# Kernel optimization log

Hardware: AMD Instinct MI355X
Metric: run time of the kernel (lower is better)

Reference implementation:

```python
import jax, jax.numpy as jnp
import numpy as np

ANGRES = 5  # u = v = angRes, n = 25


def _l2norm(x, axis):
    n = jnp.sqrt(jnp.sum(x * x, axis=axis, keepdims=True))
    return x / jnp.maximum(n, 1e-12)  # matches torch F.normalize eps


def _cos_attn(qm, km, vm):
    # qm: (b, M, K), km: (b, K, M), vm: (b, M, K)
    q = _l2norm(qm, -1)
    k = _l2norm(km, -2)
    att = jax.nn.softmax(q @ k, axis=-1)  # (b, M, M)
    return att @ vm


def _af_attn(x, u, v):  # AngularFrequencyAttention: b c (u v) h w -> b (c u) (h v w)
    b, c, n, h, w = x.shape
    t = x.reshape(b, c, u, v, h, w)
    qm = t.transpose(0, 1, 2, 4, 3, 5).reshape(b, c * u, h * v * w)   # (b,c,u,h,v,w)
    km = t.transpose(0, 4, 3, 5, 1, 2).reshape(b, h * v * w, c * u)   # (b,h,v,w,c,u)
    o = _cos_attn(qm, km, qm)
    o = o.reshape(b, c, u, h, v, w).transpose(0, 1, 2, 4, 3, 5).reshape(b, c, n, h, w)
    return o + x


def _sa_attn(x, u, v):  # SpatialAngularAttention: b c (u v) h w -> b (h u) (c v w)
    b, c, n, h, w = x.shape
    t = x.reshape(b, c, u, v, h, w)
    qm = t.transpose(0, 4, 2, 1, 3, 5).reshape(b, h * u, c * v * w)   # (b,h,u,c,v,w)
    km = t.transpose(0, 1, 3, 5, 4, 2).reshape(b, c * v * w, h * u)   # (b,c,v,w,h,u)
    o = _cos_attn(qm, km, qm)
    o = o.reshape(b, h, u, c, v, w).transpose(0, 3, 2, 4, 1, 5).reshape(b, c, n, h, w)
    return o + x


def _sf_attn(x, u, v):  # SpatialFrequencyAttention: b c (u v) h w -> b (c h) (w u v)
    b, c, n, h, w = x.shape
    t = x.reshape(b, c, u, v, h, w)
    qm = t.transpose(0, 1, 4, 5, 2, 3).reshape(b, c * h, w * u * v)   # (b,c,h,w,u,v)
    km = t.transpose(0, 5, 2, 3, 1, 4).reshape(b, w * u * v, c * h)   # (b,w,u,v,c,h)
    o = _cos_attn(qm, km, qm)
    o = o.reshape(b, c, h, w, u, v).transpose(0, 1, 4, 5, 2, 3).reshape(b, c, n, h, w)
    return o + x


def _layernorm(x, g, bta, eps=1e-5):
    mu = jnp.mean(x, -1, keepdims=True)
    var = jnp.mean(jnp.square(x - mu), -1, keepdims=True)
    return (x - mu) * jax.lax.rsqrt(var + eps) * g + bta


def setup_inputs() -> dict:
    key = jax.random.key(0)
    k0, k1, k2 = jax.random.split(key, 3)
    b, c, n, h, w = 4, 64, 25, 48, 48
    x = jax.random.normal(k0, (b, c, n, h, w), dtype=jnp.float32)
    gamma = jnp.ones((3 * c,), dtype=jnp.float32)
    beta = jnp.zeros((3 * c,), dtype=jnp.float32)
    w1 = jax.random.normal(k1, (3 * c, c), dtype=jnp.float32) * 0.02
    w2 = jax.random.normal(k2, (c, c), dtype=jnp.float32) * 0.02
    return {"x": x, "gamma": gamma, "beta": beta, "w1": w1, "w2": w2}


def reference(x, gamma, beta, w1, w2):
    u = v = ANGRES
    b, c, n, h, w = x.shape
    sf = _sf_attn(x, u, v)
    af = _af_attn(x, u, v)
    sa = _sa_attn(x, u, v)
    cat = jnp.concatenate([sf, af, sa], axis=1)            # (b, 3c, n, h, w)
    f = cat.transpose(0, 3, 4, 2, 1).reshape(b * h * w, n, 3 * c)
    y = _layernorm(f, gamma, beta)
    y = jax.nn.relu(y @ w1) @ w2                            # (bhw, n, c); dropout p=0.01 is eval-identity
    out = y.reshape(b, h, w, n, c).transpose(0, 4, 3, 1, 2) + x
    return out
```

## Files before the change

kernel.cpp:

```cpp
#include <hip/hip_runtime.h>
#include <stdint.h>

typedef __attribute__((ext_vector_type(8))) short bf16x8;
typedef __attribute__((ext_vector_type(4))) float f32x4;

__device__ __forceinline__ float b2f(short s) {
  union { unsigned u; float f; } a; a.u = ((unsigned)(unsigned short)s) << 16; return a.f;
}
__device__ __forceinline__ short f2b(float f) {
  union { float f; unsigned u; } a; a.f = f;
  unsigned r = a.u + 0x7fffu + ((a.u >> 16) & 1u);
  return (short)(r >> 16);
}
__device__ __forceinline__ void gload16(const void* g, void* l) {
  __builtin_amdgcn_global_load_lds((__attribute__((address_space(1))) void*)g,
                                   (__attribute__((address_space(3))) void*)l, 16, 0, 0);
}

#define SWZ(row, col) ((col) ^ (((row) & 7) << 3))

__global__ __launch_bounds__(256) void permute_sf_k(const float* __restrict__ x,
                                                    short* __restrict__ Q,
                                                    float* __restrict__ inv) {
  __shared__ float buf[4][1200];
  int wave = threadIdx.x >> 6, lane = threadIdx.x & 63;
  int gr = blockIdx.x * 4 + wave;
  int b = gr / 3072, m = gr - b * 3072;
  int c = m / 48, hh = m - c * 48;
  const float* xb = x + (long)(b * 64 + c) * 57600 + hh * 48;
  for (int uv = 0; uv < 25; ++uv)
    if (lane < 48) buf[wave][uv * 48 + lane] = xb[uv * 2304 + lane];
  __syncthreads();
  short* Qr = Q + (long)gr * 1280;
  float ss = 0.f;
  for (int k = lane; k < 1280; k += 64) {
    float v = 0.f;
    if (k < 1200) { int wv = k / 25, uv = k - wv * 25; v = buf[wave][uv * 48 + wv]; }
    ss += v * v;
    Qr[k] = f2b(v);
  }
  #pragma unroll
  for (int o = 32; o >= 1; o >>= 1) ss += __shfl_xor(ss, o, 64);
  if (lane == 0) inv[gr] = 1.0f / fmaxf(sqrtf(ss), 1e-12f);
}

__global__ __launch_bounds__(256) void permtr_all_k(const float* __restrict__ x,
    short* __restrict__ Qaf, short* __restrict__ QTaf,
    short* __restrict__ Qsa, short* __restrict__ QTsa,
    float* __restrict__ ssaf, float* __restrict__ sssa) {
  __shared__ short t[32][33];
  int bid = blockIdx.x;
  int isAF = (bid < 17280);
  int M, Mp, Kp, kt, mt, b;
  short *Q, *QT; float* ss;
  if (isAF) { M = 320; Mp = 384; Kp = 11520; kt = bid % 360; int r = bid / 360; mt = r % 12; b = r / 12;
              Q = Qaf; QT = QTaf; ss = ssaf; }
  else { int id = bid - 17280; M = 240; Mp = 256; Kp = 15360; kt = id % 480; int r = id / 480; mt = r % 8; b = r / 8;
         Q = Qsa; QT = QTsa; ss = sssa; }
  int k0 = kt * 32, m0 = mt * 32;
  int tx = threadIdx.x & 31, ty = threadIdx.x >> 5;
  const float* xb = x + (long)b * 3686400;
  #pragma unroll
  for (int i = 0; i < 32; i += 8) {
    int m = m0 + ty + i, k = k0 + tx;
    float v = 0.f;
    if (m < M) {
      int q1 = k / 240, r2 = k - q1 * 240;
      int v5 = r2 / 48, wv = r2 - v5 * 48;
      int a1 = m / 5, u = m - a1 * 5;
      long xi = isAF ? ((long)a1 * 25 + u * 5 + v5) * 2304 + q1 * 48 + wv
                     : ((long)q1 * 25 + u * 5 + v5) * 2304 + a1 * 48 + wv;
      v = xb[xi];
    }
    t[ty + i][tx] = f2b(v);
  }
  __syncthreads();
  long Qb = (long)b * Mp * Kp;
  #pragma unroll
  for (int i = 0; i < 32; i += 8)
    Q[Qb + (long)(m0 + ty + i) * Kp + k0 + tx] = t[ty + i][tx];
  #pragma unroll
  for (int i = 0; i < 32; i += 8)
    QT[Qb + (long)(k0 + ty + i) * Mp + m0 + tx] = t[tx][ty + i];
  if (threadIdx.x < 32 && m0 + (int)threadIdx.x < M) {
    float s = 0.f;
    #pragma unroll
    for (int k = 0; k < 32; ++k) { float f = b2f(t[threadIdx.x][k]); s += f * f; }
    atomicAdd(&ss[b * Mp + m0 + threadIdx.x], s);
  }
}

__global__ __launch_bounds__(256) void transpose_k(const short* __restrict__ in, short* __restrict__ out,
                                                   int R, int C) {
  __shared__ short t[32][33];
  long base = (long)blockIdx.z * R * C;
  int c0 = blockIdx.x * 32, r0 = blockIdx.y * 32;
  int tx = threadIdx.x & 31, ty = threadIdx.x >> 5;
  #pragma unroll
  for (int i = 0; i < 32; i += 8)
    t[ty + i][tx] = in[base + (long)(r0 + ty + i) * C + c0 + tx];
  __syncthreads();
  #pragma unroll
  for (int i = 0; i < 32; i += 8)
    out[base + (long)(c0 + ty + i) * R + r0 + tx] = t[tx][ty + i];
}

__global__ __launch_bounds__(256, 2) void gemm1_tri_k(const short* __restrict__ Q,
                                                      const float* __restrict__ invn,
                                                      short* __restrict__ att,
                                                      float* __restrict__ rowsum) {
  __shared__ short sm[32768];
  int tid = threadIdx.x, wave = tid >> 6, lane = tid & 63;
  int la = lane & 15, lb = lane >> 4;
  int bat = blockIdx.z;
  int bx = blockIdx.x, yt = 0, rem = bx;
  while (rem >= 24 - yt) { rem -= 24 - yt; ++yt; }
  int xt = yt + rem;
  const short* Qb = Q + (long)bat * 3932160L;
  const float* inv = invn + (long)bat * 3072;
  int row0 = yt * 128, col0 = xt * 128;
  f32x4 acc[4][4] = {};
  int wr = wave >> 1, wc = wave & 1;
  int rloc = tid >> 3, cbase = (tid & 7) * 8;
  int ldsoff = tid * 8;

  const short *pA[4], *pB[4];
  #pragma unroll
  for (int p = 0; p < 4; ++p) {
    int row = p * 32 + rloc;
    int sc = SWZ(row, cbase);
    pA[p] = Qb + (long)(row0 + row) * 1280 + sc;
    pB[p] = Qb + (long)(col0 + row) * 1280 + sc;
  }

  #define TRI_STAGE(KT, BUF) { \
    short* Asb = sm + (BUF) * 16384; \
    short* Bsb = Asb + 8192; \
    _Pragma("unroll") \
    for (int p = 0; p < 4; ++p) { \
      gload16(pA[p] + (KT) * 64, (void*)(Asb + p * 2048 + ldsoff)); \
      gload16(pB[p] + (KT) * 64, (void*)(Bsb + p * 2048 + ldsoff)); \
    } }
  #define TRI_COMP(BUF) { \
    const short* Asb = sm + (BUF) * 16384; \
    const short* Bsb = Asb + 8192; \
    _Pragma("unroll") \
    for (int kk = 0; kk < 64; kk += 32) { \
      bf16x8 av[4], bv[4]; \
      _Pragma("unroll") \
      for (int m = 0; m < 4; ++m) \
        av[m] = *(const bf16x8*)&Asb[(wr * 64 + m * 16 + la) * 64 + SWZ(la, kk + lb * 8)]; \
      _Pragma("unroll") \
      for (int nn = 0; nn < 4; ++nn) \
        bv[nn] = *(const bf16x8*)&Bsb[(wc * 64 + nn * 16 + la) * 64 + SWZ(la, kk + lb * 8)]; \
      _Pragma("unroll") \
      for (int m = 0; m < 4; ++m) \
        _Pragma("unroll") \
        for (int nn = 0; nn < 4; ++nn) \
          acc[m][nn] = __builtin_amdgcn_mfma_f32_16x16x32_bf16(av[m], bv[nn], acc[m][nn], 0, 0, 0); \
    } }

  TRI_STAGE(0, 0)
  for (int kt = 0; kt < 19; ++kt) {
    TRI_STAGE(kt + 1, (kt + 1) & 1)
    asm volatile("s_waitcnt vmcnt(8)" ::: "memory");
    __builtin_amdgcn_s_barrier();
    TRI_COMP(kt & 1)
    asm volatile("" ::: "memory");
    __builtin_amdgcn_s_barrier();
  }
  asm volatile("s_waitcnt vmcnt(0)" ::: "memory");
  __builtin_amdgcn_s_barrier();
  TRI_COMP(1)
  asm volatile("" ::: "memory");
  __builtin_amdgcn_s_barrier();

  short* staged = sm;
  #pragma unroll
  for (int m = 0; m < 4; ++m) {
    #pragma unroll
    for (int nn = 0; nn < 4; ++nn) {
      int cl = wc * 64 + nn * 16 + la;
      float ic = inv[col0 + cl];
      #pragma unroll
      for (int j = 0; j < 4; ++j) {
        int rl = wr * 64 + m * 16 + lb * 4 + j;
        staged[rl * 136 + cl] = f2b(__expf(acc[m][nn][j] * inv[row0 + rl] * ic));
      }
    }
  }
  __syncthreads();
  short* attb = att + (long)bat * 9437184L;
  float* rsb = rowsum + (long)bat * 3072;
  {
    int r = tid >> 1, half = tid & 1;
    short* dst = attb + (long)(row0 + r) * 3072 + col0 + half * 64;
    const short* src = &staged[r * 136 + half * 64];
    float s = 0.f;
    #pragma unroll
    for (int q = 0; q < 8; ++q) {
      bf16x8 v = *(const bf16x8*)&src[q * 8];
      *(bf16x8*)&dst[q * 8] = v;
      #pragma unroll
      for (int jj = 0; jj < 8; ++jj) s += b2f(v[jj]);
    }
    s += __shfl_xor(s, 1, 64);
    if (half == 0) atomicAdd(&rsb[row0 + r], s);
  }
  if (xt != yt) {
    int c = tid >> 1, half = tid & 1;
    short* dst = attb + (long)(col0 + c) * 3072 + row0 + half * 64;
    float s = 0.f;
    #pragma unroll
    for (int q = 0; q < 8; ++q) {
      bf16x8 o;
      #pragma unroll
      for (int jj = 0; jj < 8; ++jj) {
        o[jj] = staged[(half * 64 + q * 8 + jj) * 136 + c];
        s += b2f(o[jj]);
      }
      *(bf16x8*)&dst[q * 8] = o;
    }
    s += __shfl_xor(s, 1, 64);
    if (half == 0) atomicAdd(&rsb[col0 + c], s);
  }
}

__global__ __launch_bounds__(256, 2) void gemm_s_all_k(
    const short* __restrict__ Aaf, const short* __restrict__ Asa,
    float* __restrict__ Sfaf, float* __restrict__ Sfsa)
{
  __shared__ short sm[32768];
  int bid = blockIdx.x;
  const short* A; float* Sf;
  int lda, ktotal, ksper, ldc, row0, col0, bat, kc;
  long sA, sS;
  if (bid < 288) {
    int txy = bid % 9, z = bid / 9;
    col0 = (txy % 3) * 128; row0 = (txy / 3) * 128;
    bat = z / 8; kc = z % 8;
    lda = 11520; ktotal = 180; ksper = 23; ldc = 384;
    sA = 4423680L; sS = 147456L; A = Aaf; Sf = Sfaf;
  } else {
    int id = bid - 288;
    int txy = id % 4, z = id / 4;
    col0 = (txy % 2) * 128; row0 = (txy / 2) * 128;
    bat = z / 16; kc = z % 16;
    lda = 15360; ktotal = 240; ksper = 15; ldc = 256;
    sA = 3932160L; sS = 65536L; A = Asa; Sf = Sfsa;
  }
  int tid = threadIdx.x;
  int wave = tid >> 6, lane = tid & 63;
  int la = lane & 15, lb = lane >> 4;
  const short* Ab = A + (long)bat * sA;
  int kb = kc * ksper, ke = min(ktotal, kb + ksper);
  int L = ke - kb;
  f32x4 acc[4][4] = {};
  int wr = wave >> 1, wc = wave & 1;
  int rloc = tid >> 3, cbase = (tid & 7) * 8;
  int ldsoff = tid * 8;

  const short *pA[4], *pB[4];
  #pragma unroll
  for (int p = 0; p < 4; ++p) {
    int row = p * 32 + rloc;
    int sc = SWZ(row, cbase);
    pA[p] = Ab + (long)(row0 + row) * lda + sc;
    pB[p] = Ab + (long)(col0 + row) * lda + sc;
  }

  #define GS_STAGE(KT, BUF) { \
    short* Asb = sm + (BUF) * 16384; \
    short* Bsb = Asb + 8192; \
    _Pragma("unroll") \
    for (int p = 0; p < 4; ++p) { \
      gload16(pA[p] + (KT) * 64, (void*)(Asb + p * 2048 + ldsoff)); \
      gload16(pB[p] + (KT) * 64, (void*)(Bsb + p * 2048 + ldsoff)); \
    } }
  #define GS_COMP(BUF) { \
    const short* Asb = sm + (BUF) * 16384; \
    const short* Bsb = Asb + 8192; \
    _Pragma("unroll") \
    for (int kk = 0; kk < 64; kk += 32) { \
      bf16x8 av[4], bv[4]; \
      _Pragma("unroll") \
      for (int m = 0; m < 4; ++m) \
        av[m] = *(const bf16x8*)&Asb[(wr * 64 + m * 16 + la) * 64 + SWZ(la, kk + lb * 8)]; \
      _Pragma("unroll") \
      for (int nn = 0; nn < 4; ++nn) \
        bv[nn] = *(const bf16x8*)&Bsb[(wc * 64 + nn * 16 + la) * 64 + SWZ(la, kk + lb * 8)]; \
      _Pragma("unroll") \
      for (int m = 0; m < 4; ++m) \
        _Pragma("unroll") \
        for (int nn = 0; nn < 4; ++nn) \
          acc[m][nn] = __builtin_amdgcn_mfma_f32_16x16x32_bf16(av[m], bv[nn], acc[m][nn], 0, 0, 0); \
    } }

  GS_STAGE(kb, 0)
  for (int t = 0; t < L - 1; ++t) {
    GS_STAGE(kb + t + 1, (t + 1) & 1)
    asm volatile("s_waitcnt vmcnt(8)" ::: "memory");
    __builtin_amdgcn_s_barrier();
    GS_COMP(t & 1)
    asm volatile("" ::: "memory");
    __builtin_amdgcn_s_barrier();
  }
  asm volatile("s_waitcnt vmcnt(0)" ::: "memory");
  __builtin_amdgcn_s_barrier();
  GS_COMP((L - 1) & 1)

  float* Sb = Sf + (long)bat * sS;
  #pragma unroll
  for (int m = 0; m < 4; ++m) {
    int gr0 = row0 + wr * 64 + m * 16 + lb * 4;
    #pragma unroll
    for (int nn = 0; nn < 4; ++nn) {
      int gc = col0 + wc * 64 + nn * 16 + la;
      #pragma unroll
      for (int j = 0; j < 4; ++j)
        atomicAdd(&Sb[(long)(gr0 + j) * ldc + gc], acc[m][nn][j]);
    }
  }
}

__global__ __launch_bounds__(256) void softmax_all_k(
    const float* __restrict__ Sfaf, const float* __restrict__ Sfsa,
    const float* __restrict__ ssaf, const float* __restrict__ sssa,
    short* __restrict__ attaf, short* __restrict__ attsa)
{
  int wave = threadIdx.x >> 6, lane = threadIdx.x & 63;
  int rid = blockIdx.x * 4 + wave;
  int row, b, Mv, Mp; const float *Sf, *ss; short* att;
  if (rid < 1280) { row = rid % 320; b = rid / 320; Mv = 320; Mp = 384; Sf = Sfaf; ss = ssaf; att = attaf; }
  else { int id = rid - 1280; row = id % 240; b = id / 240; Mv = 240; Mp = 256; Sf = Sfsa; ss = sssa; att = attsa; }
  long sS = (long)Mp * Mp;
  const float* Sr = Sf + (long)b * sS + (long)row * Mp;
  const float* ssb = ss + b * Mp;
  float inv_i = rsqrtf(fmaxf(ssb[row], 1e-24f));
  float ev[6] = {0.f, 0.f, 0.f, 0.f, 0.f, 0.f};
  float sum = 0.f;
  #pragma unroll
  for (int q = 0; q < 6; ++q) {
    int j = q * 64 + lane;
    if (j < Mv) {
      float e = __expf(Sr[j] * inv_i * rsqrtf(fmaxf(ssb[j], 1e-24f)));
      ev[q] = e; sum += e;
    }
  }
  #pragma unroll
  for (int o = 32; o >= 1; o >>= 1) sum += __shfl_xor(sum, o, 64);
  float rden = 1.0f / sum;
  short* ar = att + (long)b * sS + (long)row * Mp;
  #pragma unroll
  for (int q = 0; q < 6; ++q) {
    int j = q * 64 + lane;
    if (j < Mp) ar[j] = (j < Mv) ? f2b(ev[q] * rden) : (short)0;
  }
}

__global__ __launch_bounds__(512) void gemm2sf_k(const short* __restrict__ A,
                                                 const short* __restrict__ B,
                                                 const float* __restrict__ rowsum,
                                                 short* __restrict__ F) {
  __shared__ short sm[65536];
  int tid = threadIdx.x;
  int wave = tid >> 6, lane = tid & 63;
  int la = lane & 15, lb = lane >> 4;
  int wr = wave >> 2, wc = wave & 3;
  int wk;
  { int xcd = blockIdx.x & 7, j = blockIdx.x >> 3; wk = xcd * 30 + j; }
  int yt = wk % 12, rem = wk / 12;
  int xt = rem % 5, bat = rem / 5;
  const short* Ab = A + (long)bat * 9437184L;
  const short* Bb = B + (long)bat * 3932160L;
  int rloc = tid >> 3;
  int cbase = (tid & 7) * 8;
  int sc = cbase ^ ((rloc & 7) << 3);
  const short *pAg[4], *pBg[4];
  #pragma unroll
  for (int g = 0; g < 4; ++g) {
    pAg[g] = Ab + (long)(rloc * 48 + yt * 4 + g) * 3072 + sc;
    pBg[g] = Bb + (long)(xt * 256 + g * 64 + rloc) * 3072 + sc;
  }
  f32x4 acc[8][4] = {};

  #pragma unroll
  for (int g = 0; g < 4; ++g) {
    gload16(pAg[g], (void*)(sm + g * 4096 + tid * 8));
    gload16(pBg[g], (void*)(sm + 16384 + g * 4096 + tid * 8));
  }
  asm volatile("s_waitcnt vmcnt(0)" ::: "memory");
  __builtin_amdgcn_s_barrier();

  #define G2_PHASE(MH, KK, LOADB) { \
    if (LOADB) { \
      _Pragma("unroll") \
      for (int nn = 0; nn < 4; ++nn) \
        bv[nn] = *(const bf16x8*)&Bsb[(wc * 64 + nn * 16 + la) * 64 + SWZ(la, (KK) + lb * 8)]; \
    } \
    _Pragma("unroll") \
    for (int m = 0; m < 4; ++m) \
      av[m] = *(const bf16x8*)&Asb[(wr * 128 + (MH) * 64 + m * 16 + la) * 64 + SWZ(la, (KK) + lb * 8)]; \
    __builtin_amdgcn_s_setprio(1); \
    _Pragma("unroll") \
    for (int m = 0; m < 4; ++m) \
      _Pragma("unroll") \
      for (int nn = 0; nn < 4; ++nn) \
        acc[(MH) * 4 + m][nn] = __builtin_amdgcn_mfma_f32_16x16x32_bf16(av[m], bv[nn], acc[(MH) * 4 + m][nn], 0, 0, 0); \
    __builtin_amdgcn_s_setprio(0); \
  }

  for (int t = 0; t < 48; ++t) {
    const short* Asb = sm + (t & 1) * 32768;
    const short* Bsb = Asb + 16384;
    short* An = sm + ((t + 1) & 1) * 32768;
    short* Bn = An + 16384;
    int k1 = (t + 1) * 64;
    bool pf = (t < 47);
    bf16x8 av[4], bv[4];

    asm volatile("s_waitcnt vmcnt(2)" ::: "memory");
    __builtin_amdgcn_s_barrier();
    if (pf) { gload16(pBg[0] + k1, (void*)(Bn + tid * 8));
              gload16(pBg[1] + k1, (void*)(Bn + 4096 + tid * 8)); }
    G2_PHASE(0, 0, 1)
    asm volatile("s_waitcnt vmcnt(2)" ::: "memory");
    __builtin_amdgcn_s_barrier();
    if (pf) { gload16(pBg[2] + k1, (void*)(Bn + 8192 + tid * 8));
              gload16(pBg[3] + k1, (void*)(Bn + 12288 + tid * 8)); }
    G2_PHASE(1, 0, 0)
    asm volatile("s_waitcnt vmcnt(4)" ::: "memory");
    __builtin_amdgcn_s_barrier();
    if (pf) { gload16(pAg[0] + k1, (void*)(An + tid * 8));
              gload16(pAg[2] + k1, (void*)(An + 8192 + tid * 8)); }
    G2_PHASE(0, 32, 1)
    asm volatile("s_waitcnt vmcnt(6)" ::: "memory");
    __builtin_amdgcn_s_barrier();
    if (pf) { gload16(pAg[1] + k1, (void*)(An + 4096 + tid * 8));
              gload16(pAg[3] + k1, (void*)(An + 12288 + tid * 8)); }
    G2_PHASE(1, 32, 0)
  }
  __syncthreads();

  const float* rsb = rowsum + (long)bat * 3072;
  float rs[8][4];
  #pragma unroll
  for (int m = 0; m < 8; ++m) {
    int sub = wr * 2 + (m >> 2);
    #pragma unroll
    for (int j = 0; j < 4; ++j) {
      int cc = (m & 3) * 16 + lb * 4 + j;
      rs[m][j] = 1.0f / rsb[cc * 48 + yt * 4 + sub];
    }
  }
  short* staged = sm;
  #pragma unroll
  for (int m = 0; m < 8; ++m) {
    int sub = wr * 2 + (m >> 2);
    #pragma unroll
    for (int nn = 0; nn < 4; ++nn) {
      int gcl = wc * 64 + nn * 16 + la;
      int chunk = gcl * 4 + sub;
      int key = (gcl & 7) << 3;
      short4 o;
      o.x = f2b(acc[m][nn][0] * rs[m][0]); o.y = f2b(acc[m][nn][1] * rs[m][1]);
      o.z = f2b(acc[m][nn][2] * rs[m][2]); o.w = f2b(acc[m][nn][3] * rs[m][3]);
      *(short4*)&staged[chunk * 64 + (((m & 3) * 16 + lb * 4) ^ key)] = o;
    }
  }
  __syncthreads();
  #pragma unroll
  for (int i = 0; i < 16; ++i) {
    int chunk = i * 64 + (tid >> 3);
    int part = tid & 7;
    int gcl = chunk >> 2, sub = chunk & 3;
    int key = (gcl & 7) << 3;
    bf16x8 v = *(const bf16x8*)&staged[chunk * 64 + ((part * 8) ^ key)];
    int gc = xt * 256 + gcl;
    if (gc < 1200) {
      int hh = yt * 4 + sub;
      int wv = gc / 25, nidx = gc - wv * 25;
      long base = (((long)(bat * 48 + hh) * 48 + wv) * 25 + nidx) * 192 + part * 8;
      *(bf16x8*)&F[base] = v;
    }
  }
}

__global__ __launch_bounds__(256) void gemm2_afsa_k(
    const short* __restrict__ attaf, const short* __restrict__ QTaf,
    const short* __restrict__ attsa, const short* __restrict__ QTsa,
    short* __restrict__ F)
{
  __shared__ short sm[20480];
  short* As = sm;
  short* Bs = sm + 4096;
  int bid = blockIdx.x;
  int isAF = (bid < 900);
  int NX, NY, LDA, KST, wk;
  const short *A, *B; long SA, SB;
  if (isAF) {
    NX = 45; NY = 5; LDA = 384; KST = 6; SA = 147456L; SB = 4423680L; A = attaf; B = QTaf;
    int xcd = bid & 7, j = bid >> 3;
    wk = (xcd < 4) ? xcd * 113 + j : 4 * 113 + (xcd - 4) * 112 + j;
  } else {
    NX = 60; NY = 4; LDA = 256; KST = 4; SA = 65536L; SB = 3932160L; A = attsa; B = QTsa;
    int id = bid - 900;
    int xcd = id & 7, j = id >> 3;
    wk = xcd * 120 + j;
  }
  int yt = wk % NY, rem = wk / NY;
  int xt = rem % NX, bat = rem / NX;
  int tid = threadIdx.x, wave = tid >> 6, lane = tid & 63;
  int la = lane & 15, lb = lane >> 4;
  const short* Ab = A + (long)bat * SA;
  const short* Bb = B + (long)bat * SB;
  f32x4 acc[4][4] = {};
  int rloc = tid >> 3, cbase = (tid & 7) * 8;
  int ldsoff = tid * 8;

  const short *pA[2], *pB[8];
  #pragma unroll
  for (int p = 0; p < 2; ++p) {
    int r = p * 32 + rloc;
    int sc = SWZ(r, cbase);
    int rowg = isAF ? (r * 5 + yt) : (yt * 64 + r);
    pA[p] = Ab + (long)rowg * LDA + sc;
  }
  #pragma unroll
  for (int p = 0; p < 8; ++p) {
    int rb = p * 32 + rloc;
    int sc = SWZ(rb, cbase);
    int rowg;
    if (isAF) rowg = xt * 256 + rb;
    else { int c = rb & 63, g = rb >> 6; rowg = c * 240 + xt * 4 + g; }
    pB[p] = Bb + (long)rowg * LDA + sc;
  }

  for (int kt = 0; kt < KST; ++kt) {
    #pragma unroll
    for (int p = 0; p < 2; ++p)
      gload16(pA[p] + kt * 64, (void*)(As + p * 2048 + ldsoff));
    #pragma unroll
    for (int p = 0; p < 8; ++p)
      gload16(pB[p] + kt * 64, (void*)(Bs + p * 2048 + ldsoff));
    __syncthreads();
    #pragma unroll
    for (int kk = 0; kk < 64; kk += 32) {
      bf16x8 av[4], bv[4];
      #pragma unroll
      for (int m = 0; m < 4; ++m)
        av[m] = *(const bf16x8*)&As[(m * 16 + la) * 64 + SWZ(la, kk + lb * 8)];
      #pragma unroll
      for (int nn = 0; nn < 4; ++nn)
        bv[nn] = *(const bf16x8*)&Bs[(wave * 64 + nn * 16 + la) * 64 + SWZ(la, kk + lb * 8)];
      #pragma unroll
      for (int m = 0; m < 4; ++m)
        #pragma unroll
        for (int nn = 0; nn < 4; ++nn)
          acc[m][nn] = __builtin_amdgcn_mfma_f32_16x16x32_bf16(av[m], bv[nn], acc[m][nn], 0, 0, 0);
    }
    __syncthreads();
  }

  short* staged = sm;
  #pragma unroll
  for (int m = 0; m < 4; ++m) {
    #pragma unroll
    for (int nn = 0; nn < 4; ++nn) {
      if (!isAF) {
        #pragma unroll
        for (int j = 0; j < 4; ++j)
          staged[((m * 16 + lb * 4 + j) * 4 + wave) * 72 + nn * 16 + la] = f2b(acc[m][nn][j]);
      } else {
        short4 o;
        o.x = f2b(acc[m][nn][0]); o.y = f2b(acc[m][nn][1]);
        o.z = f2b(acc[m][nn][2]); o.w = f2b(acc[m][nn][3]);
        *(short4*)&staged[(wave * 64 + nn * 16 + la) * 72 + m * 16 + lb * 4] = o;
      }
    }
  }
  __syncthreads();

  #pragma unroll
  for (int rd = 0; rd < 8; ++rd) {
    int chunk = rd * 32 + (tid >> 3);
    int part = tid & 7;
    bf16x8 v = *(const bf16x8*)&staged[chunk * 72 + part * 8];
    long base; bool ok = true;
    if (isAF) {
      int gc = xt * 256 + chunk;
      int hh = gc / 240, r2 = gc - hh * 240, v5 = r2 / 48, wv = r2 - v5 * 48;
      base = (((long)(bat * 48 + hh) * 48 + wv) * 25 + yt * 5 + v5) * 192 + 64 + part * 8;
    } else {
      int r = chunk >> 2, g = chunk & 3;
      int gr = yt * 64 + r; ok = (gr < 240);
      int hh = gr / 5, u = gr - hh * 5;
      int r2 = xt * 4 + g, v5 = r2 / 48, wv = r2 - v5 * 48;
      base = (((long)(bat * 48 + hh) * 48 + wv) * 25 + u * 5 + v5) * 192 + 128 + part * 8;
    }
    if (ok) *(bf16x8*)&F[base] = v;
  }
}

__global__ __launch_bounds__(256) void prep_w_k(const float* __restrict__ w1, const float* __restrict__ w2,
                                                short* __restrict__ w1t, short* __restrict__ w2t) {
  int idx = blockIdx.x * 256 + threadIdx.x;
  if (idx < 12288) {
    int i = idx / 64, j = idx - i * 64;
    w1t[j * 192 + i] = f2b(w1[idx]);
  } else if (idx < 16384) {
    int k = idx - 12288;
    int i = k / 64, j = k - i * 64;
    w2t[j * 64 + i] = f2b(w2[k]);
  }
}

__global__ __launch_bounds__(256) void ln_mlp_mfma_k(
    const short* __restrict__ F, const float* __restrict__ x,
    const float* __restrict__ gamma, const float* __restrict__ beta,
    const short* __restrict__ w1t, const short* __restrict__ w2t,
    float* __restrict__ out)
{
  int n = blockIdx.x, hh = blockIdx.y, b = blockIdx.z;
  __shared__ short A1[48 * 200];
  __shared__ float xs[64 * 49];
  __shared__ __align__(16) char pool[19584];
  short* Fs = (short*)pool;
  short* Y1 = (short*)pool;
  float* Y2 = (float*)(pool + 6912);
  int tid = threadIdx.x, wave = tid >> 6, lane = tid & 63;
  int la = lane & 15, lb = lane >> 4;
  long Fb0 = ((long)(b * 48 + hh) * 1200 + n) * 192;
  long xb = (long)b * 3686400 + (long)n * 2304 + hh * 48;

  #pragma unroll
  for (int it = 0; it < 5; ++it) {
    int ci = tid + 256 * it;
    if (ci < 1152) {
      int r = ci / 24, q = ci - r * 24;
      gload16(&F[Fb0 + (long)r * 4800 + q * 8], (void*)(Fs + ci * 8));
    }
  }
  {
    int ch = tid >> 2, qq = tid & 3;
    const float* xr = x + xb + (long)ch * 57600 + qq * 12;
    #pragma unroll
    for (int i = 0; i < 12; ++i) xs[ch * 49 + qq * 12 + i] = xr[i];
  }
  __syncthreads();

  float g0 = gamma[lane], g1 = gamma[lane + 64], g2 = gamma[lane + 128];
  float bt0 = beta[lane], bt1 = beta[lane + 64], bt2 = beta[lane + 128];
  #pragma unroll 4
  for (int rr = 0; rr < 12; ++rr) {
    int r = wave * 12 + rr;
    float xv = xs[lane * 49 + r];
    float v0 = b2f(Fs[r * 192 + lane]) + xv;
    float v1 = b2f(Fs[r * 192 + lane + 64]) + xv;
    float v2 = b2f(Fs[r * 192 + lane + 128]) + xv;
    float s = v0 + v1 + v2;
    #pragma unroll
    for (int o = 32; o >= 1; o >>= 1) s += __shfl_xor(s, o, 64);
    float mu = s * (1.f / 192.f);
    float d0 = v0 - mu, d1 = v1 - mu, d2 = v2 - mu;
    float q = d0 * d0 + d1 * d1 + d2 * d2;
    #pragma unroll
    for (int o = 32; o >= 1; o >>= 1) q += __shfl_xor(q, o, 64);
    float rsq = rsqrtf(q * (1.f / 192.f) + 1e-5f);
    A1[r * 200 + lane]       = f2b(d0 * rsq * g0 + bt0);
    A1[r * 200 + lane + 64]  = f2b(d1 * rsq * g1 + bt1);
    A1[r * 200 + lane + 128] = f2b(d2 * rsq * g2 + bt2);
  }
  __syncthreads();

  f32x4 acc1[3] = {};
  #pragma unroll
  for (int ks = 0; ks < 6; ++ks) {
    bf16x8 bv = *(const bf16x8*)&w1t[(wave * 16 + la) * 192 + ks * 32 + lb * 8];
    #pragma unroll
    for (int m = 0; m < 3; ++m) {
      bf16x8 av = *(const bf16x8*)&A1[(m * 16 + la) * 200 + ks * 32 + lb * 8];
      acc1[m] = __builtin_amdgcn_mfma_f32_16x16x32_bf16(av, bv, acc1[m], 0, 0, 0);
    }
  }
  #pragma unroll
  for (int m = 0; m < 3; ++m)
    #pragma unroll
    for (int j = 0; j < 4; ++j)
      Y1[(m * 16 + lb * 4 + j) * 72 + wave * 16 + la] = f2b(fmaxf(acc1[m][j], 0.f));
  __syncthreads();

  f32x4 acc2[3] = {};
  #pragma unroll
  for (int ks = 0; ks < 2; ++ks) {
    bf16x8 bv = *(const bf16x8*)&w2t[(wave * 16 + la) * 64 + ks * 32 + lb * 8];
    #pragma unroll
    for (int m = 0; m < 3; ++m) {
      bf16x8 av = *(const bf16x8*)&Y1[(m * 16 + la) * 72 + ks * 32 + lb * 8];
      acc2[m] = __builtin_amdgcn_mfma_f32_16x16x32_bf16(av, bv, acc2[m], 0, 0, 0);
    }
  }
  #pragma unroll
  for (int m = 0; m < 3; ++m)
    #pragma unroll
    for (int j = 0; j < 4; ++j)
      Y2[(m * 16 + lb * 4 + j) * 66 + wave * 16 + la] = acc2[m][j];
  __syncthreads();

  #pragma unroll
  for (int i = 0; i < 12; ++i) {
    int e = tid + 256 * i;
    int cc = e / 48, wv = e - cc * 48;
    out[xb + (long)cc * 57600 + wv] = Y2[wv * 66 + cc] + xs[cc * 49 + wv];
  }
}

extern "C" void kernel_launch(void* const* d_in, const int* in_sizes, int n_in,
                              void* d_out, int out_size, void* d_ws, size_t ws_size,
                              hipStream_t stream) {
  (void)in_sizes; (void)n_in; (void)out_size;
  const float* x     = (const float*)d_in[0];
  const float* gamma = (const float*)d_in[1];
  const float* beta  = (const float*)d_in[2];
  const float* w1    = (const float*)d_in[3];
  const float* w2    = (const float*)d_in[4];
  float* out = (float*)d_out;

  const size_t NEED = 237191168UL;
  if (ws_size < NEED) return;
  char* ws = (char*)d_ws;
  short* F     = (short*)(ws);
  short* attsf = (short*)(ws + 88473600UL);
  short* Qsf   = (short*)(ws + 163971072UL);
  short* QTsf  = (short*)(ws + 199360512UL);
  float* rowsum = (float*)(ws + 234749952UL);
  float* invn  = (float*)(ws + 237109248UL);
  short* w1t   = (short*)(ws + 237158400UL);
  short* w2t   = (short*)(ws + 237182976UL);
  short* Qaf   = (short*)(ws + 88473600UL);
  short* QTaf  = (short*)(ws + 123863040UL);
  float* Sfsa  = (float*)(ws + 159252480UL);
  float* ssaf  = (float*)(ws + 160301056UL);
  float* sssa  = (float*)(ws + 160307200UL);
  short* attaf = (short*)(ws + 160311296UL);
  short* attsa = (short*)(ws + 161490944UL);
  short* Qsa   = (short*)(ws + 163971072UL);
  short* QTsa  = (short*)(ws + 195428352UL);
  float* Sfaf  = (float*)(ws + 234749952UL);

  prep_w_k<<<64, 256, 0, stream>>>(w1, w2, w1t, w2t);

  permute_sf_k<<<3072, 256, 0, stream>>>(x, Qsf, invn);
  transpose_k<<<dim3(40, 96, 4), 256, 0, stream>>>(Qsf, QTsf, 3072, 1280);
  hipMemsetAsync(rowsum, 0, 49152, stream);
  gemm1_tri_k<<<dim3(300, 1, 4), 256, 0, stream>>>(Qsf, invn, attsf, rowsum);
  gemm2sf_k<<<dim3(240), 512, 0, stream>>>(attsf, QTsf, rowsum, F);

  hipMemsetAsync(Sfaf, 0, 2359296, stream);
  hipMemsetAsync(Sfsa, 0, 1048576, stream);
  hipMemsetAsync(ssaf, 0, 10240, stream);
  permtr_all_k<<<32640, 256, 0, stream>>>(x, Qaf, QTaf, Qsa, QTsa, ssaf, sssa);
  gemm_s_all_k<<<544, 256, 0, stream>>>(Qaf, Qsa, Sfaf, Sfsa);
  softmax_all_k<<<560, 256, 0, stream>>>(Sfaf, Sfsa, ssaf, sssa, attaf, attsa);
  gemm2_afsa_k<<<1860, 256, 0, stream>>>(attaf, QTaf, attsa, QTsa, F);

  ln_mlp_mfma_k<<<dim3(25, 48, 4), 256, 0, stream>>>(F, x, gamma, beta, w1t, w2t, out);
}
```

Measured before the change: 466.5 us.

## Fuse SF permute, transpose, norm and rowsum zeroing into one kernel

Replaces the per-row SF permute kernel, the separate bf16 transpose kernel and the rowsum memset with a single kernel per (batch, channel). It stages the whole 48x1200 slab in LDS and writes both Q and QT from there. The Sfsa and ssaf memsets are merged into one contiguous memset, and the final gemm2 iteration now waits with vmcnt(0). This removes a global round trip of Q for the transpose and two launches. In exchange it uses a large LDS footprint (about 123KB), runs only 256 blocks, and writes QT in strided 96-byte chunks.

```diff
diff --git a/kernel.cpp b/kernel.cpp
--- a/kernel.cpp
+++ b/kernel.cpp
@@ -19,29 +19,52 @@
 
 #define SWZ(row, col) ((col) ^ (((row) & 7) << 3))
 
-__global__ __launch_bounds__(256) void permute_sf_k(const float* __restrict__ x,
-                                                    short* __restrict__ Q,
-                                                    float* __restrict__ inv) {
-  __shared__ float buf[4][1200];
-  int wave = threadIdx.x >> 6, lane = threadIdx.x & 63;
-  int gr = blockIdx.x * 4 + wave;
-  int b = gr / 3072, m = gr - b * 3072;
-  int c = m / 48, hh = m - c * 48;
-  const float* xb = x + (long)(b * 64 + c) * 57600 + hh * 48;
-  for (int uv = 0; uv < 25; ++uv)
-    if (lane < 48) buf[wave][uv * 48 + lane] = xb[uv * 2304 + lane];
-  __syncthreads();
-  short* Qr = Q + (long)gr * 1280;
-  float ss = 0.f;
-  for (int k = lane; k < 1280; k += 64) {
-    float v = 0.f;
-    if (k < 1200) { int wv = k / 25, uv = k - wv * 25; v = buf[wave][uv * 48 + wv]; }
-    ss += v * v;
-    Qr[k] = f2b(v);
-  }
-  #pragma unroll
-  for (int o = 32; o >= 1; o >>= 1) ss += __shfl_xor(ss, o, 64);
-  if (lane == 0) inv[gr] = 1.0f / fmaxf(sqrtf(ss), 1e-12f);
+__global__ __launch_bounds__(256) void permute_sf2_k(const float* __restrict__ x,
+                                                     short* __restrict__ Q,
+                                                     short* __restrict__ QT,
+                                                     float* __restrict__ inv,
+                                                     float* __restrict__ rowsum) {
+  __shared__ short kw[48 * 1288];
+  __shared__ float ssrow[48];
+  int tid = threadIdx.x;
+  int c = blockIdx.x, b = blockIdx.y;
+  int bid = b * 64 + c;
+  if (tid < 48) { rowsum[bid * 48 + tid] = 0.f; ssrow[tid] = 0.f; }
+  for (int e = tid; e < 48 * 88; e += 256) {
+    int r = e / 88, q = e - r * 88;
+    kw[r * 1288 + 1200 + q] = 0;
+  }
+  const float* xp = x + ((long)(b * 64 + c)) * 57600;
+  for (int i = 0; i < 225; ++i) {
+    int e = tid + 256 * i;
+    int uv = e / 2304, r2 = e - uv * 2304;
+    int hh = r2 / 48, w = r2 - hh * 48;
+    kw[hh * 1288 + w * 25 + uv] = f2b(xp[e]);
+  }
+  __syncthreads();
+  long qb = ((long)b * 3072 + c * 48) * 1280;
+  for (int ci2 = tid; ci2 < 7680; ci2 += 256) {
+    int r = ci2 / 160, q = ci2 - r * 160;
+    bf16x8 v = *(const bf16x8*)&kw[r * 1288 + q * 8];
+    *(bf16x8*)&Q[qb + (long)r * 1280 + q * 8] = v;
+    float s = 0.f;
+    #pragma unroll
+    for (int j = 0; j < 8; ++j) { float f = b2f(v[j]); s += f * f; }
+    atomicAdd(&ssrow[r], s);
+  }
+  __syncthreads();
+  if (tid < 48)
+    inv[(long)b * 3072 + c * 48 + tid] = 1.0f / fmaxf(sqrtf(ssrow[tid]), 1e-12f);
+  long qtb = (long)b * 3932160L + (long)c * 48;
+  for (int k = tid; k < 1280; k += 256) {
+    short tmp[48];
+    #pragma unroll
+    for (int r = 0; r < 48; ++r) tmp[r] = kw[r * 1288 + k];
+    short* dst = &QT[qtb + (long)k * 3072];
+    #pragma unroll
+    for (int q = 0; q < 6; ++q)
+      *(bf16x8*)&dst[q * 8] = *(const bf16x8*)&tmp[q * 8];
+  }
 }
 
 __global__ __launch_bounds__(256) void permtr_all_k(const float* __restrict__ x,
@@ -88,21 +111,6 @@
     for (int k = 0; k < 32; ++k) { float f = b2f(t[threadIdx.x][k]); s += f * f; }
     atomicAdd(&ss[b * Mp + m0 + threadIdx.x], s);
   }
-}
-
-__global__ __launch_bounds__(256) void transpose_k(const short* __restrict__ in, short* __restrict__ out,
-                                                   int R, int C) {
-  __shared__ short t[32][33];
-  long base = (long)blockIdx.z * R * C;
-  int c0 = blockIdx.x * 32, r0 = blockIdx.y * 32;
-  int tx = threadIdx.x & 31, ty = threadIdx.x >> 5;
-  #pragma unroll
-  for (int i = 0; i < 32; i += 8)
-    t[ty + i][tx] = in[base + (long)(r0 + ty + i) * C + c0 + tx];
-  __syncthreads();
-  #pragma unroll
-  for (int i = 0; i < 32; i += 8)
-    out[base + (long)(c0 + ty + i) * R + r0 + tx] = t[tx][ty + i];
 }
 
 __global__ __launch_bounds__(256, 2) void gemm1_tri_k(const short* __restrict__ Q,
@@ -424,7 +432,8 @@
     if (pf) { gload16(pBg[0] + k1, (void*)(Bn + tid * 8));
               gload16(pBg[1] + k1, (void*)(Bn + 4096 + tid * 8)); }
     G2_PHASE(0, 0, 1)
-    asm volatile("s_waitcnt vmcnt(2)" ::: "memory");
+    if (pf) asm volatile("s_waitcnt vmcnt(2)" ::: "memory");
+    else    asm volatile("s_waitcnt vmcnt(0)" ::: "memory");
     __builtin_amdgcn_s_barrier();
     if (pf) { gload16(pBg[2] + k1, (void*)(Bn + 8192 + tid * 8));
               gload16(pBg[3] + k1, (void*)(Bn + 12288 + tid * 8)); }
@@ -750,15 +759,12 @@
 
   prep_w_k<<<64, 256, 0, stream>>>(w1, w2, w1t, w2t);
 
-  permute_sf_k<<<3072, 256, 0, stream>>>(x, Qsf, invn);
-  transpose_k<<<dim3(40, 96, 4), 256, 0, stream>>>(Qsf, QTsf, 3072, 1280);
-  hipMemsetAsync(rowsum, 0, 49152, stream);
+  permute_sf2_k<<<dim3(64, 4), 256, 0, stream>>>(x, Qsf, QTsf, invn, rowsum);
   gemm1_tri_k<<<dim3(300, 1, 4), 256, 0, stream>>>(Qsf, invn, attsf, rowsum);
   gemm2sf_k<<<dim3(240), 512, 0, stream>>>(attsf, QTsf, rowsum, F);
 
   hipMemsetAsync(Sfaf, 0, 2359296, stream);
-  hipMemsetAsync(Sfsa, 0, 1048576, stream);
-  hipMemsetAsync(ssaf, 0, 10240, stream);
+  hipMemsetAsync((char*)Sfsa, 0, 1058816, stream);
   permtr_all_k<<<32640, 256, 0, stream>>>(x, Qaf, QTaf, Qsa, QTsa, ssaf, sssa);
   gemm_s_all_k<<<544, 256, 0, stream>>>(Qaf, Qsa, Sfaf, Sfsa);
   softmax_all_k<<<560, 256, 0, stream>>>(Sfaf, Sfsa, ssaf, sssa, attaf, attsa);
```

Result: slower. 478.6 us (+2.6%).
